# Optimization experiments

Hardware: AMD Instinct MI355X
Metric: run time of the kernel (lower is better)

The kernel has to match this reference:

```python
import jax, jax.numpy as jnp
import numpy as np

EMBED_DIM = 1024
NUM_HEADS = 16
PROJ_DIM = EMBED_DIM // NUM_HEADS


def setup_inputs() -> dict:
    key = jax.random.key(0)
    ks = jax.random.split(key, 11)
    B, S, D = 2, 2048, EMBED_DIM
    scale = 1.0 / np.sqrt(D)
    inp = {
        'q': jax.random.normal(ks[0], (B, S, D), jnp.float32),
        'k': jax.random.normal(ks[1], (B, S, D), jnp.float32),
        'v': jax.random.normal(ks[2], (B, S, D), jnp.float32),
        'Wq': jax.random.normal(ks[3], (D, D), jnp.float32) * scale,
        'bq': jnp.zeros((D,), jnp.float32),
        'Wk': jax.random.normal(ks[4], (D, D), jnp.float32) * scale,
        'bk': jnp.zeros((D,), jnp.float32),
        'Wv': jax.random.normal(ks[5], (D, D), jnp.float32) * scale,
        'bv': jnp.zeros((D,), jnp.float32),
        'Wo': jax.random.normal(ks[6], (D, D), jnp.float32) * scale,
        'bo': jnp.zeros((D,), jnp.float32),
        'use_causal_mask': 1,
    }
    return inp


def _split_heads(x, B):
    # [B, S, D] -> [B, H, S, Pd]
    return x.reshape(B, -1, NUM_HEADS, PROJ_DIM).transpose(0, 2, 1, 3)


def reference(q, k, v, Wq, bq, Wk, bk, Wv, bv, Wo, bo, use_causal_mask):
    B, S, D = q.shape
    qh = _split_heads(q @ Wq + bq, B)
    kh = _split_heads(k @ Wk + bk, B)
    vh = _split_heads(v @ Wv + bv, B)
    # scaled dot-product attention; scores [B, H, S, S]
    logits = jnp.einsum('bhqd,bhkd->bhqk', qh, kh) / jnp.sqrt(
        jnp.asarray(PROJ_DIM, jnp.float32))
    if use_causal_mask:
        # faithful to source: logits += log(tril * 1e-9 + 1e-9)
        tril = jnp.tril(jnp.ones((S, S), dtype=logits.dtype))
        logits = logits + jnp.log(tril * 1e-9 + 1e-9)
    attn = jax.nn.softmax(logits, axis=-1)
    out = jnp.einsum('bhqk,bhkd->bhqd', attn, vh)
    out = out.transpose(0, 2, 1, 3).reshape(B, S, D)
    return out @ Wo + bo
```

## Files before the change

### kernel.cpp

```cpp
#include <hip/hip_runtime.h>
#include <hip/hip_bf16.h>
#include <stdint.h>

#define EMBED 1024
#define NH    16
#define PD    64
#define BATCH 2
#define SEQ   2048

typedef unsigned short u16;
typedef __attribute__((ext_vector_type(8))) short bf16x8;
typedef __attribute__((ext_vector_type(4))) float f32x4;

#define WAITALL() __builtin_amdgcn_s_waitcnt(0)

__device__ __forceinline__ float b2f(u16 x) {
  unsigned u = ((unsigned)x) << 16;
  return __builtin_bit_cast(float, u);
}
__device__ __forceinline__ u16 f2b(float x) {
  unsigned u = __builtin_bit_cast(unsigned, x);
  u += 0x7fffu + ((u >> 16) & 1u);
  return (u16)(u >> 16);
}
__device__ __forceinline__ float loadIn(const void* p, size_t i, int isf32) {
  return isf32 ? ((const float*)p)[i] : b2f(((const u16*)p)[i]);
}
__device__ __forceinline__ void async16(const void* g, void* l) {
  __builtin_amdgcn_global_load_lds((const __attribute__((address_space(1))) void*)g,
                                   (__attribute__((address_space(3))) void*)l,
                                   16, 0, 0);
}

__global__ void detect(const unsigned* q, int* flag) {
  int lane = threadIdx.x;
  unsigned lo = q[lane] & 0xffffu;
  unsigned e = (lo >> 7) & 0xffu;
  int pred = (e >= 110 && e <= 135);
  unsigned long long m = __ballot(pred);
  if (lane == 0) flag[0] = (__popcll(m) < 32) ? 1 : 0;
}

__global__ __launch_bounds__(256) void conv_qkv(const void* q, const void* k,
                                                const void* v, u16* qb, u16* kb,
                                                u16* vb, const int* flag) {
  const int isf32 = flag[0];
  size_t i = ((size_t)blockIdx.x * 256 + threadIdx.x) * 8;
  const void* src = (blockIdx.y == 0) ? q : (blockIdx.y == 1) ? k : v;
  u16* dst = (blockIdx.y == 0) ? qb : (blockIdx.y == 1) ? kb : vb;
  u16 tmp[8];
  if (isf32) {
    const float* s = (const float*)src + i;
    float4 a = *(const float4*)s;
    float4 b = *(const float4*)(s + 4);
    tmp[0] = f2b(a.x); tmp[1] = f2b(a.y); tmp[2] = f2b(a.z); tmp[3] = f2b(a.w);
    tmp[4] = f2b(b.x); tmp[5] = f2b(b.y); tmp[6] = f2b(b.z); tmp[7] = f2b(b.w);
  } else {
    const uint4 r = *(const uint4*)((const u16*)src + i);
    *(uint4*)tmp = r;
  }
  *(uint4*)(dst + i) = *(uint4*)tmp;
}

__global__ __launch_bounds__(256) void conv_w(const void* Wq, const void* Wk,
                                              const void* Wv, const void* Wo,
                                              u16* out, const int* flag) {
  const int isf32 = flag[0];
  const void* W = (blockIdx.z == 0) ? Wq : (blockIdx.z == 1) ? Wk
                : (blockIdx.z == 2) ? Wv : Wo;
  u16* WT = out + (size_t)blockIdx.z * EMBED * EMBED;
  __shared__ float sh[64][65];
  int r0 = blockIdx.y * 64, c0 = blockIdx.x * 64;
  int col = threadIdx.x & 63;
  int rb  = threadIdx.x >> 6;
#pragma unroll
  for (int i = 0; i < 16; i++) {
    int row = i * 4 + rb;
    sh[row][col] = loadIn(W, (size_t)(r0 + row) * EMBED + c0 + col, isf32);
  }
  __syncthreads();
#pragma unroll
  for (int i = 0; i < 16; i++) {
    int row = i * 4 + rb;
    WT[(size_t)(c0 + row) * EMBED + r0 + col] = f2b(sh[col][row]);
  }
}

__device__ __forceinline__ void gemm_core(const u16* __restrict__ A,
                                          const u16* __restrict__ Bt,
                                          int tm, int tn, u16* lds,
                                          f32x4 acc[4][4]) {
  const int tid = threadIdx.x;
  const int lane = tid & 63;
  const int wv = tid >> 6;
  const int wm = (wv >> 1) * 64, wn = (wv & 1) * 64;
  const int l15 = lane & 15, quad = lane >> 4;
  const int rbx = (lane & 7) << 3;
  u16* As = lds;
  u16* Bs = lds + 128 * 64;
  f32x4 z = {0.f, 0.f, 0.f, 0.f};
#pragma unroll
  for (int i = 0; i < 4; i++)
#pragma unroll
    for (int j = 0; j < 4; j++) acc[i][j] = z;

  for (int kt = 0; kt < EMBED; kt += 64) {
#pragma unroll
    for (int i = 0; i < 4; i++) {
      int c = i * 256 + tid;
      int row = c >> 3;
      int col = ((c & 7) << 3) ^ ((row & 7) << 3);
      async16(A + (size_t)(tm + row) * EMBED + kt + col, As + c * 8);
      async16(Bt + (size_t)(tn + row) * EMBED + kt + col, Bs + c * 8);
    }
    WAITALL();
    __syncthreads();
#pragma unroll
    for (int ks = 0; ks < 64; ks += 32) {
      int ko = (ks + quad * 8) ^ rbx;
      bf16x8 af[4], bf[4];
#pragma unroll
      for (int mt = 0; mt < 4; mt++)
        af[mt] = *(const bf16x8*)(As + (wm + mt * 16 + l15) * 64 + ko);
#pragma unroll
      for (int nt = 0; nt < 4; nt++)
        bf[nt] = *(const bf16x8*)(Bs + (wn + nt * 16 + l15) * 64 + ko);
#pragma unroll
      for (int mt = 0; mt < 4; mt++)
#pragma unroll
        for (int nt = 0; nt < 4; nt++)
          acc[mt][nt] = __builtin_amdgcn_mfma_f32_16x16x32_bf16(
              af[mt], bf[nt], acc[mt][nt], 0, 0, 0);
    }
    WAITALL();
    __syncthreads();
  }
}

__global__ __launch_bounds__(256) void qkv_gemm(
    const u16* qb, const u16* kb, const u16* vb, const u16* wts,
    const void* bq, const void* bk, const void* bv,
    u16* Qh, u16* Kh, u16* Vt, const int* flag) {
  __shared__ __align__(16) u16 lds[2 * 128 * 64];
  const int isf32 = flag[0];
  int z = blockIdx.z;
  const u16* A = (z == 0) ? qb : (z == 1) ? kb : vb;
  const u16* Bt = wts + (size_t)z * EMBED * EMBED;
  const void* bias = (z == 0) ? bq : (z == 1) ? bk : bv;
  int tm = blockIdx.y * 128, tn = blockIdx.x * 128;
  f32x4 acc[4][4];
  gemm_core(A, Bt, tm, tn, lds, acc);

  int lane = threadIdx.x & 63, wv = threadIdx.x >> 6;
  int wm = (wv >> 1) * 64, wn = (wv & 1) * 64;
  int rbase = tm + wm + ((lane >> 4) << 2);
  int cbase = tn + wn + (lane & 15);
  if (z < 2) {
    u16* dst = (z == 0) ? Qh : Kh;
#pragma unroll
    for (int mt = 0; mt < 4; mt++)
#pragma unroll
      for (int nt = 0; nt < 4; nt++) {
        int col = cbase + nt * 16;
        float bv_ = loadIn(bias, col, isf32);
        int h = col >> 6, p = col & 63;
#pragma unroll
        for (int j = 0; j < 4; j++) {
          int row = rbase + mt * 16 + j;
          int b = row >> 11, s = row & 2047;
          dst[(((size_t)(b * NH + h) * SEQ) + s) * PD + p] =
              f2b(acc[mt][nt][j] + bv_);
        }
      }
  } else {
#pragma unroll
    for (int mt = 0; mt < 4; mt++)
#pragma unroll
      for (int nt = 0; nt < 4; nt++) {
        int col = cbase + nt * 16;
        float bv_ = loadIn(bias, col, isf32);
        int h = col >> 6, p = col & 63;
        int row0 = rbase + mt * 16;
        int b = row0 >> 11, s0 = row0 & 2047;
        ushort4 pk;
        pk.x = f2b(acc[mt][nt][0] + bv_);
        pk.y = f2b(acc[mt][nt][1] + bv_);
        pk.z = f2b(acc[mt][nt][2] + bv_);
        pk.w = f2b(acc[mt][nt][3] + bv_);
        *(ushort4*)(Vt + ((size_t)(b * NH + h) * PD + p) * SEQ + s0) = pk;
      }
  }
}

__global__ __launch_bounds__(256) void attn(const u16* __restrict__ Qh,
                                            const u16* __restrict__ Kh,
                                            const u16* __restrict__ Vt,
                                            u16* __restrict__ O,
                                            const int* __restrict__ maskflag) {
  __shared__ __align__(16) u16 Qs[128 * 64];
  __shared__ __align__(16) u16 Ks[64 * 64];
  __shared__ __align__(16) u16 Vs[64 * 64];
  const int bh = blockIdx.y;
  const int qt = blockIdx.x * 128;
  const int tid = threadIdx.x, lane = tid & 63, wv = tid >> 6;
  const int l15 = lane & 15, quad = lane >> 4;
  const int rbx = (lane & 7) << 3;
  const size_t head = (size_t)bh * SEQ * PD;
  const bool causal = (maskflag[0] != 0);
  const float C = 0.18033688011112042f;

#pragma unroll
  for (int i = 0; i < 4; i++) {
    int c = i * 256 + tid;
    int row = c >> 3;
    int col = ((c & 7) << 3) ^ ((row & 7) << 3);
    async16(Qh + head + (size_t)(qt + row) * PD + col, Qs + c * 8);
  }

  float lacc[2] = {0.f, 0.f};
  f32x4 oacc[4][2];
  f32x4 z4 = {0.f, 0.f, 0.f, 0.f};
#pragma unroll
  for (int mt = 0; mt < 4; mt++)
#pragma unroll
    for (int n = 0; n < 2; n++) oacc[mt][n] = z4;

  const int rowq = qt + wv * 32;

  for (int t = 0; t < SEQ / 64; t++) {
    const int k0 = t * 64;
#pragma unroll
    for (int i = 0; i < 2; i++) {
      int c = i * 256 + tid;
      int row = c >> 3;
      int col = ((c & 7) << 3) ^ ((row & 7) << 3);
      async16(Kh + head + (size_t)(k0 + row) * PD + col, Ks + c * 8);
      async16(Vt + head + (size_t)row * SEQ + k0 + col, Vs + c * 8);
    }
    WAITALL();
    __syncthreads();

    f32x4 st[4][2];
#pragma unroll
    for (int kt = 0; kt < 4; kt++)
#pragma unroll
      for (int n = 0; n < 2; n++) st[kt][n] = z4;
#pragma unroll
    for (int ks = 0; ks < 64; ks += 32) {
      int ko = (ks + quad * 8) ^ rbx;
      bf16x8 qf[2];
      qf[0] = *(const bf16x8*)(Qs + (wv * 32 + l15) * 64 + ko);
      qf[1] = *(const bf16x8*)(Qs + (wv * 32 + 16 + l15) * 64 + ko);
#pragma unroll
      for (int kt = 0; kt < 4; kt++) {
        bf16x8 kf = *(const bf16x8*)(Ks + (kt * 16 + l15) * 64 + ko);
        st[kt][0] = __builtin_amdgcn_mfma_f32_16x16x32_bf16(kf, qf[0], st[kt][0], 0, 0, 0);
        st[kt][1] = __builtin_amdgcn_mfma_f32_16x16x32_bf16(kf, qf[1], st[kt][1], 0, 0, 0);
      }
    }

    const int mode = !causal ? 0 : (k0 > qt + 127 ? 2 : (k0 + 63 <= qt ? 0 : 1));
    const float ub = (mode == 2) ? -17.f : -16.f;
    unsigned pw[2][2][4];
#pragma unroll
    for (int kt = 0; kt < 4; kt++) {
#pragma unroll
      for (int n = 0; n < 2; n++) {
        const int qrow = rowq + n * 16 + l15;
        float p[4];
#pragma unroll
        for (int r = 0; r < 4; r++) {
          float bias = ub;
          if (mode == 1) {
            int kappa = k0 + kt * 16 + 4 * quad + r;
            bias = (kappa > qrow) ? -17.f : -16.f;
          }
          p[r] = exp2f(fmaf(st[kt][n][r], C, bias));
          lacc[n] += p[r];
        }
        pw[kt >> 1][n][(kt & 1) * 2 + 0] =
            (unsigned)f2b(p[0]) | ((unsigned)f2b(p[1]) << 16);
        pw[kt >> 1][n][(kt & 1) * 2 + 1] =
            (unsigned)f2b(p[2]) | ((unsigned)f2b(p[3]) << 16);
      }
    }

#pragma unroll
    for (int p = 0; p < 2; p++) {
      bf16x8 pf[2];
      pf[0] = __builtin_bit_cast(bf16x8,
          (uint4){pw[p][0][0], pw[p][0][1], pw[p][0][2], pw[p][0][3]});
      pf[1] = __builtin_bit_cast(bf16x8,
          (uint4){pw[p][1][0], pw[p][1][1], pw[p][1][2], pw[p][1][3]});
#pragma unroll
      for (int mt = 0; mt < 4; mt++) {
        int row = mt * 16 + l15;
        int sz = (row & 7) << 3;
        int c1 = (p * 32 + 4 * quad) ^ sz;
        int c2 = (p * 32 + 16 + 4 * quad) ^ sz;
        ushort4 a = *(const ushort4*)(Vs + row * 64 + c1);
        ushort4 bb = *(const ushort4*)(Vs + row * 64 + c2);
        bf16x8 vf = {(short)a.x, (short)a.y, (short)a.z, (short)a.w,
                     (short)bb.x, (short)bb.y, (short)bb.z, (short)bb.w};
        oacc[mt][0] = __builtin_amdgcn_mfma_f32_16x16x32_bf16(vf, pf[0], oacc[mt][0], 0, 0, 0);
        oacc[mt][1] = __builtin_amdgcn_mfma_f32_16x16x32_bf16(vf, pf[1], oacc[mt][1], 0, 0, 0);
      }
    }
    WAITALL();
    __syncthreads();
  }

#pragma unroll
  for (int n = 0; n < 2; n++) {
    lacc[n] += __shfl_xor(lacc[n], 16, 64);
    lacc[n] += __shfl_xor(lacc[n], 32, 64);
  }
  float inv[2] = {1.f / lacc[0], 1.f / lacc[1]};

  const int b = bh >> 4, h = bh & 15;
#pragma unroll
  for (int mt = 0; mt < 4; mt++) {
#pragma unroll
    for (int n = 0; n < 2; n++) {
      int qrow = rowq + n * 16 + l15;
      ushort4 w;
      w.x = f2b(oacc[mt][n][0] * inv[n]);
      w.y = f2b(oacc[mt][n][1] * inv[n]);
      w.z = f2b(oacc[mt][n][2] * inv[n]);
      w.w = f2b(oacc[mt][n][3] * inv[n]);
      *(ushort4*)(O + ((size_t)b * SEQ + qrow) * EMBED + h * PD + mt * 16 +
                  4 * quad) = w;
    }
  }
}

__global__ __launch_bounds__(256) void out_gemm(const u16* __restrict__ Ob,
                                                const u16* __restrict__ WoT,
                                                const void* __restrict__ bo,
                                                void* __restrict__ out,
                                                const int* __restrict__ flag) {
  __shared__ __align__(16) u16 lds[2 * 128 * 64];
  const int isf32 = flag[0];
  int tm = blockIdx.y * 128, tn = blockIdx.x * 128;
  f32x4 acc[4][4];
  gemm_core(Ob, WoT, tm, tn, lds, acc);
  int lane = threadIdx.x & 63, wv = threadIdx.x >> 6;
  int wm = (wv >> 1) * 64, wn = (wv & 1) * 64;
  int rbase = tm + wm + ((lane >> 4) << 2);
  int cbase = tn + wn + (lane & 15);
#pragma unroll
  for (int mt = 0; mt < 4; mt++)
#pragma unroll
    for (int nt = 0; nt < 4; nt++) {
      int col = cbase + nt * 16;
      float bv_ = loadIn(bo, col, isf32);
#pragma unroll
      for (int j = 0; j < 4; j++) {
        int row = rbase + mt * 16 + j;
        float val = acc[mt][nt][j] + bv_;
        size_t off = (size_t)row * EMBED + col;
        if (isf32) ((float*)out)[off] = val;
        else       ((u16*)out)[off]   = f2b(val);
      }
    }
}

extern "C" void kernel_launch(void* const* d_in, const int* in_sizes, int n_in,
                              void* d_out, int out_size, void* d_ws, size_t ws_size,
                              hipStream_t stream) {
  const void* q  = d_in[0];
  const void* k  = d_in[1];
  const void* v  = d_in[2];
  const void* Wq = d_in[3];
  const void* bq = d_in[4];
  const void* Wk = d_in[5];
  const void* bk = d_in[6];
  const void* Wv = d_in[7];
  const void* bv = d_in[8];
  const void* Wo = d_in[9];
  const void* bo = d_in[10];
  const int* msk = (const int*)d_in[11];

  char* ws = (char*)d_ws;
  int*  flag  = (int*)ws;
  u16*  qb    = (u16*)(ws + 64);
  u16*  kb    = qb + (size_t)4194304;
  u16*  vb    = kb + (size_t)4194304;
  u16*  WT    = vb + (size_t)4194304;
  u16*  Qh    = WT + (size_t)4194304;
  u16*  Kh    = Qh + (size_t)4194304;
  u16*  Vt    = Kh + (size_t)4194304;
  u16*  Ob    = Vt + (size_t)4194304;

  detect<<<1, 64, 0, stream>>>((const unsigned*)q, flag);
  conv_qkv<<<dim3(2048, 3), 256, 0, stream>>>(q, k, v, qb, kb, vb, flag);
  conv_w<<<dim3(16, 16, 4), 256, 0, stream>>>(Wq, Wk, Wv, Wo, WT, flag);
  qkv_gemm<<<dim3(8, 32, 3), 256, 0, stream>>>(qb, kb, vb, WT, bq, bk, bv,
                                               Qh, Kh, Vt, flag);
  attn<<<dim3(16, 32), 256, 0, stream>>>(Qh, Kh, Vt, Ob, msk);
  out_gemm<<<dim3(8, 32), 256, 0, stream>>>(Ob, WT + (size_t)3 * 1048576,
                                            bo, d_out, flag);
}
```

Before: 302.9 us.

## Permute V layout for single 16B LDS reads, hoist Q fragments, use native bf16 cvt

The V projection epilogue now writes Vt with a permuted sequence order inside each 32-element block. This lets the attention kernel load each V MFMA operand as one 16-byte LDS read instead of two 8-byte reads plus a repack. Q fragments are loaded into registers once before the KV loop instead of on every tile, and the row-sum accumulation is rebalanced into a tree. The manual round-to-nearest bf16 conversion is replaced by the compiler's __bf16 cast, which may lower to hardware convert instructions. The combined Vt write and read permutation must stay consistent, and hoisting Q adds register pressure.

```diff
diff --git a/kernel.cpp b/kernel.cpp
--- a/kernel.cpp
+++ b/kernel.cpp
@@ -18,10 +18,9 @@
   unsigned u = ((unsigned)x) << 16;
   return __builtin_bit_cast(float, u);
 }
-__device__ __forceinline__ u16 f2b(float x) {
-  unsigned u = __builtin_bit_cast(unsigned, x);
-  u += 0x7fffu + ((u >> 16) & 1u);
-  return (u16)(u >> 16);
+__device__ __forceinline__ u16 cvtb(float x) {
+  __bf16 h = (__bf16)x;
+  return __builtin_bit_cast(u16, h);
 }
 __device__ __forceinline__ float loadIn(const void* p, size_t i, int isf32) {
   return isf32 ? ((const float*)p)[i] : b2f(((const u16*)p)[i]);
@@ -53,8 +52,8 @@
     const float* s = (const float*)src + i;
     float4 a = *(const float4*)s;
     float4 b = *(const float4*)(s + 4);
-    tmp[0] = f2b(a.x); tmp[1] = f2b(a.y); tmp[2] = f2b(a.z); tmp[3] = f2b(a.w);
-    tmp[4] = f2b(b.x); tmp[5] = f2b(b.y); tmp[6] = f2b(b.z); tmp[7] = f2b(b.w);
+    tmp[0] = cvtb(a.x); tmp[1] = cvtb(a.y); tmp[2] = cvtb(a.z); tmp[3] = cvtb(a.w);
+    tmp[4] = cvtb(b.x); tmp[5] = cvtb(b.y); tmp[6] = cvtb(b.z); tmp[7] = cvtb(b.w);
   } else {
     const uint4 r = *(const uint4*)((const u16*)src + i);
     *(uint4*)tmp = r;
@@ -82,7 +81,7 @@
 #pragma unroll
   for (int i = 0; i < 16; i++) {
     int row = i * 4 + rb;
-    WT[(size_t)(c0 + row) * EMBED + r0 + col] = f2b(sh[col][row]);
+    WT[(size_t)(c0 + row) * EMBED + r0 + col] = cvtb(sh[col][row]);
   }
 }
 
@@ -169,7 +168,7 @@
           int row = rbase + mt * 16 + j;
           int b = row >> 11, s = row & 2047;
           dst[(((size_t)(b * NH + h) * SEQ) + s) * PD + p] =
-              f2b(acc[mt][nt][j] + bv_);
+              cvtb(acc[mt][nt][j] + bv_);
         }
       }
   } else {
@@ -182,12 +181,14 @@
         int h = col >> 6, p = col & 63;
         int row0 = rbase + mt * 16;
         int b = row0 >> 11, s0 = row0 & 2047;
+        int beta = s0 >> 5, w = s0 & 31;
+        int pos = (beta << 5) + (((w >> 2) & 3) << 3) + ((w >> 4) << 2);
         ushort4 pk;
-        pk.x = f2b(acc[mt][nt][0] + bv_);
-        pk.y = f2b(acc[mt][nt][1] + bv_);
-        pk.z = f2b(acc[mt][nt][2] + bv_);
-        pk.w = f2b(acc[mt][nt][3] + bv_);
-        *(ushort4*)(Vt + ((size_t)(b * NH + h) * PD + p) * SEQ + s0) = pk;
+        pk.x = cvtb(acc[mt][nt][0] + bv_);
+        pk.y = cvtb(acc[mt][nt][1] + bv_);
+        pk.z = cvtb(acc[mt][nt][2] + bv_);
+        pk.w = cvtb(acc[mt][nt][3] + bv_);
+        *(ushort4*)(Vt + ((size_t)(b * NH + h) * PD + p) * SEQ + pos) = pk;
       }
   }
 }
@@ -216,6 +217,15 @@
     int col = ((c & 7) << 3) ^ ((row & 7) << 3);
     async16(Qh + head + (size_t)(qt + row) * PD + col, Qs + c * 8);
   }
+  WAITALL();
+  __syncthreads();
+  bf16x8 qf[2][2];
+#pragma unroll
+  for (int ks = 0; ks < 2; ks++) {
+    int ko = (ks * 32 + quad * 8) ^ rbx;
+    qf[ks][0] = *(const bf16x8*)(Qs + (wv * 32 + l15) * 64 + ko);
+    qf[ks][1] = *(const bf16x8*)(Qs + (wv * 32 + 16 + l15) * 64 + ko);
+  }
 
   float lacc[2] = {0.f, 0.f};
   f32x4 oacc[4][2];
@@ -246,16 +256,13 @@
 #pragma unroll
       for (int n = 0; n < 2; n++) st[kt][n] = z4;
 #pragma unroll
-    for (int ks = 0; ks < 64; ks += 32) {
-      int ko = (ks + quad * 8) ^ rbx;
-      bf16x8 qf[2];
-      qf[0] = *(const bf16x8*)(Qs + (wv * 32 + l15) * 64 + ko);
-      qf[1] = *(const bf16x8*)(Qs + (wv * 32 + 16 + l15) * 64 + ko);
+    for (int ks = 0; ks < 2; ks++) {
+      int ko = (ks * 32 + quad * 8) ^ rbx;
 #pragma unroll
       for (int kt = 0; kt < 4; kt++) {
         bf16x8 kf = *(const bf16x8*)(Ks + (kt * 16 + l15) * 64 + ko);
-        st[kt][0] = __builtin_amdgcn_mfma_f32_16x16x32_bf16(kf, qf[0], st[kt][0], 0, 0, 0);
-        st[kt][1] = __builtin_amdgcn_mfma_f32_16x16x32_bf16(kf, qf[1], st[kt][1], 0, 0, 0);
+        st[kt][0] = __builtin_amdgcn_mfma_f32_16x16x32_bf16(kf, qf[ks][0], st[kt][0], 0, 0, 0);
+        st[kt][1] = __builtin_amdgcn_mfma_f32_16x16x32_bf16(kf, qf[ks][1], st[kt][1], 0, 0, 0);
       }
     }
 
@@ -276,12 +283,12 @@
             bias = (kappa > qrow) ? -17.f : -16.f;
           }
           p[r] = exp2f(fmaf(st[kt][n][r], C, bias));
-          lacc[n] += p[r];
         }
+        lacc[n] += (p[0] + p[1]) + (p[2] + p[3]);
         pw[kt >> 1][n][(kt & 1) * 2 + 0] =
-            (unsigned)f2b(p[0]) | ((unsigned)f2b(p[1]) << 16);
+            (unsigned)cvtb(p[0]) | ((unsigned)cvtb(p[1]) << 16);
         pw[kt >> 1][n][(kt & 1) * 2 + 1] =
-            (unsigned)f2b(p[2]) | ((unsigned)f2b(p[3]) << 16);
+            (unsigned)cvtb(p[2]) | ((unsigned)cvtb(p[3]) << 16);
       }
     }
 
@@ -295,13 +302,8 @@
 #pragma unroll
       for (int mt = 0; mt < 4; mt++) {
         int row = mt * 16 + l15;
-        int sz = (row & 7) << 3;
-        int c1 = (p * 32 + 4 * quad) ^ sz;
-        int c2 = (p * 32 + 16 + 4 * quad) ^ sz;
-        ushort4 a = *(const ushort4*)(Vs + row * 64 + c1);
-        ushort4 bb = *(const ushort4*)(Vs + row * 64 + c2);
-        bf16x8 vf = {(short)a.x, (short)a.y, (short)a.z, (short)a.w,
-                     (short)bb.x, (short)bb.y, (short)bb.z, (short)bb.w};
+        int chunk = ((p << 2) + quad) ^ (row & 7);
+        bf16x8 vf = *(const bf16x8*)(Vs + row * 64 + (chunk << 3));
         oacc[mt][0] = __builtin_amdgcn_mfma_f32_16x16x32_bf16(vf, pf[0], oacc[mt][0], 0, 0, 0);
         oacc[mt][1] = __builtin_amdgcn_mfma_f32_16x16x32_bf16(vf, pf[1], oacc[mt][1], 0, 0, 0);
       }
@@ -324,10 +326,10 @@
     for (int n = 0; n < 2; n++) {
       int qrow = rowq + n * 16 + l15;
       ushort4 w;
-      w.x = f2b(oacc[mt][n][0] * inv[n]);
-      w.y = f2b(oacc[mt][n][1] * inv[n]);
-      w.z = f2b(oacc[mt][n][2] * inv[n]);
-      w.w = f2b(oacc[mt][n][3] * inv[n]);
+      w.x = cvtb(oacc[mt][n][0] * inv[n]);
+      w.y = cvtb(oacc[mt][n][1] * inv[n]);
+      w.z = cvtb(oacc[mt][n][2] * inv[n]);
+      w.w = cvtb(oacc[mt][n][3] * inv[n]);
       *(ushort4*)(O + ((size_t)b * SEQ + qrow) * EMBED + h * PD + mt * 16 +
                   4 * quad) = w;
     }
@@ -360,7 +362,7 @@
         float val = acc[mt][nt][j] + bv_;
         size_t off = (size_t)row * EMBED + col;
         if (isf32) ((float*)out)[off] = val;
-        else       ((u16*)out)[off]   = f2b(val);
+        else       ((u16*)out)[off]   = cvtb(val);
       }
     }
 }
```

New measurement: 307.5 us. About the same (+1.5%).
